# Kernel optimization log

Measured on AMD Instinct MI355X. Metric: run time of the kernel, lower is better.

## Reference

```python
import jax, jax.numpy as jnp
import numpy as np
import math

N = 8192
D = 512

def setup_inputs() -> dict:
    key = jax.random.key(0)
    k1, k2, k3, k4, k5 = jax.random.split(key, 5)
    x = jax.random.normal(k1, (N, D), dtype=jnp.float32)
    mask = jax.random.randint(k2, (N, N), 0, 2) == 1
    s = 1.0 / math.sqrt(D)
    Wq = jax.random.normal(k3, (D, D), dtype=jnp.float32) * s
    Wk = jax.random.normal(k4, (D, D), dtype=jnp.float32) * s
    Wv = jax.random.normal(k5, (D, D), dtype=jnp.float32) * s
    return {"x": x, "mask": mask, "Wq": Wq, "Wk": Wk, "Wv": Wv}

def reference(x, mask, Wq, Wk, Wv):
    d_model = x.shape[-1]
    # torch nn.Linear: y = x @ W^T
    Q = x @ Wq.T
    K = x @ Wk.T
    V = x @ Wv.T
    scores = (Q @ K.T) / jnp.sqrt(jnp.asarray(d_model, x.dtype))  # [N, N]
    scores = jnp.where(mask, jnp.asarray(-1e9, x.dtype), scores)
    # manual stable softmax, matching the original op sequence
    scores = jnp.exp(scores - jnp.max(scores, axis=1, keepdims=True))
    attn = scores / jnp.sum(scores, axis=-1, keepdims=True)
    cntx = attn @ V
    return (cntx, attn)
```

## Files before the change

### kernel.cpp

```cpp
#include <hip/hip_runtime.h>

#define NTOK 8192
#define DMODEL 512
#define NWORDS 128
#define ESTRIDE (2 * NTOK)

typedef _Float16 f16;
typedef _Float16 f16x4 __attribute__((ext_vector_type(4)));
typedef _Float16 f16x8 __attribute__((ext_vector_type(8)));
typedef float f32x4 __attribute__((ext_vector_type(4)));
typedef unsigned long long u64;

__device__ __forceinline__ void async_ld16(const void* g, void* l) {
  __builtin_amdgcn_global_load_lds((const __attribute__((address_space(1))) void*)g,
                                   (__attribute__((address_space(3))) void*)l, 16, 0, 0);
}

__global__ void pack_f16(const float* __restrict__ s, f16* __restrict__ d, int n) {
  int i = (blockIdx.x * 256 + threadIdx.x) * 4;
  if (i >= n) return;
  float4 v = *(const float4*)(s + i);
  f16x4 h; h.x = (f16)v.x; h.y = (f16)v.y; h.z = (f16)v.z; h.w = (f16)v.w;
  *(f16x4*)(d + i) = h;
}

__global__ __launch_bounds__(256) void pack_mask(const int* __restrict__ mask,
                                                 u64* __restrict__ bits) {
  int wave = (blockIdx.x * 256 + threadIdx.x) >> 6;
  int lane = threadIdx.x & 63;
  size_t W0 = (size_t)wave * 8;
#pragma unroll
  for (int i = 0; i < 8; ++i) {
    int m = mask[(W0 + i) * 64 + lane];
    u64 b = __ballot(m != 0);
    if (lane == 0) bits[W0 + i] = b;
  }
}

__global__ __launch_bounds__(256) void transpose_f16(const f16* __restrict__ src,
                                                     f16* __restrict__ dst) {
  __shared__ f16 T[64][72];
  int t = threadIdx.x;
  int tok0 = blockIdx.x * 64, d0 = blockIdx.y * 64;
#pragma unroll
  for (int i = 0; i < 2; ++i) {
    int row = (t >> 3) + i * 32;
    int col = (t & 7) * 8;
    f16x8 v = *(const f16x8*)(src + (size_t)(tok0 + row) * DMODEL + d0 + col);
    *(f16x8*)(&T[row][col]) = v;
  }
  __syncthreads();
#pragma unroll
  for (int i = 0; i < 2; ++i) {
    int od = (t >> 3) + i * 32;
    int ot = (t & 7) * 8;
    f16x8 v;
#pragma unroll
    for (int j = 0; j < 8; ++j) v[j] = T[ot + j][od];
    *(f16x8*)(dst + (size_t)(d0 + od) * NTOK + tok0 + ot) = v;
  }
}

__device__ __forceinline__ void stage128x64(const f16* G, int r0, int k0, int rs,
                                            f16* lds, int t) {
  int wv = t >> 6;
  const f16* g = G + (size_t)(r0 + (t >> 3)) * rs + k0 + (t & 7) * 8;
#pragma unroll
  for (int i = 0; i < 4; ++i)
    async_ld16(g + (size_t)i * 32 * rs, (char*)lds + i * 4096 + wv * 1024);
}

template <int RS>
__device__ __forceinline__ void gemm128(const f16* A, const f16* B, int m0, int n0,
                                        f16* As, f16* Bs, int t, f32x4 (&acc)[4][4]) {
  int lane = t & 63, wv = t >> 6, quad = lane >> 4, l15 = lane & 15;
  int m_off = (wv & 1) * 64, n_off = (wv >> 1) * 64;
  for (int kt = 0; kt < RS; kt += 64) {
    __syncthreads();
    stage128x64(A, m0, kt, RS, As, t);
    stage128x64(B, n0, kt, RS, Bs, t);
    __syncthreads();
#pragma unroll
    for (int ks = 0; ks < 2; ++ks) {
      f16x8 af[4], bf[4];
#pragma unroll
      for (int mt = 0; mt < 4; ++mt)
        af[mt] = *(const f16x8*)(As + (m_off + mt * 16 + l15) * 64 + ks * 32 + quad * 8);
#pragma unroll
      for (int nt = 0; nt < 4; ++nt)
        bf[nt] = *(const f16x8*)(Bs + (n_off + nt * 16 + l15) * 64 + ks * 32 + quad * 8);
#pragma unroll
      for (int mt = 0; mt < 4; ++mt)
#pragma unroll
        for (int nt = 0; nt < 4; ++nt)
          acc[mt][nt] = __builtin_amdgcn_mfma_f32_16x16x32_f16(af[mt], bf[nt], acc[mt][nt], 0, 0, 0);
    }
  }
}

__global__ __launch_bounds__(256) void qkv_gemm(const f16* __restrict__ X,
                                                const f16* __restrict__ Wall,
                                                f16* __restrict__ Out) {
  __shared__ f16 As[128 * 64];
  __shared__ f16 Bs[128 * 64];
  int t = threadIdx.x;
  int z = blockIdx.z;
  const f16* B = Wall + (size_t)z * DMODEL * DMODEL;
  f16* C = Out + (size_t)z * NTOK * DMODEL;
  int m0 = blockIdx.y * 128, n0 = blockIdx.x * 128;
  int lane = t & 63, wv = t >> 6, quad = lane >> 4, l15 = lane & 15;
  int m_off = (wv & 1) * 64, n_off = (wv >> 1) * 64;
  f32x4 acc[4][4] = {};
  gemm128<DMODEL>(X, B, m0, n0, As, Bs, t, acc);
#pragma unroll
  for (int mt = 0; mt < 4; ++mt)
#pragma unroll
    for (int nt = 0; nt < 4; ++nt)
#pragma unroll
      for (int r = 0; r < 4; ++r) {
        int row = m0 + m_off + mt * 16 + quad * 4 + r;
        int col = n0 + n_off + nt * 16 + l15;
        C[(size_t)row * DMODEL + col] = (f16)acc[mt][nt][r];
      }
}

__global__ __launch_bounds__(256) void scores2(const f16* __restrict__ Q,
                                               const f16* __restrict__ Kh,
                                               const u64* __restrict__ bits,
                                               f16* __restrict__ Eh,
                                               float* __restrict__ rowsum) {
  __shared__ f16 SM[128 * 128];
  f16* As = SM;
  f16* Bs = SM + 128 * 64;
  int t = threadIdx.x;
  int m0 = blockIdx.y * 128, n0 = blockIdx.x * 128;
  int lane = t & 63, wv = t >> 6, quad = lane >> 4, l15 = lane & 15;
  int m_off = (wv & 1) * 64, n_off = (wv >> 1) * 64;
  f32x4 acc[4][4] = {};
  gemm128<DMODEL>(Q, Kh, m0, n0, As, Bs, t, acc);
  const float scale = 0.044194173824159216f;
  __syncthreads();
#pragma unroll
  for (int mt = 0; mt < 4; ++mt)
#pragma unroll
    for (int r = 0; r < 4; ++r) {
      int lrow = m_off + mt * 16 + quad * 4 + r;
      int row = m0 + lrow;
      u64 w = bits[(size_t)row * NWORDS + ((n0 + n_off) >> 6)];
      float rs = 0.f;
#pragma unroll
      for (int nt = 0; nt < 4; ++nt) {
        float s = acc[mt][nt][r] * scale;
        float e = ((w >> (nt * 16 + l15)) & 1) ? 0.f : __expf(s);
        rs += e;
        int col = n_off + nt * 16 + l15;
        int phys = (((col >> 3) ^ (lrow & 15)) << 3) | (col & 7);
        SM[lrow * 128 + phys] = (f16)e;
      }
      rs += __shfl_xor(rs, 1);
      rs += __shfl_xor(rs, 2);
      rs += __shfl_xor(rs, 4);
      rs += __shfl_xor(rs, 8);
      if (l15 == 0) atomicAdd(&rowsum[row], rs);
    }
  __syncthreads();
#pragma unroll
  for (int p = 0; p < 8; ++p) {
    int lrow = p * 16 + (t >> 4);
    int cb = t & 15;
    f16x8 v = *(const f16x8*)(SM + lrow * 128 + ((cb ^ (lrow & 15)) << 3));
    *(f16x8*)(Eh + (size_t)(m0 + lrow) * ESTRIDE + n0 + cb * 8) = v;
  }
}

__global__ __launch_bounds__(512, 2) void pv_kernel(const f16* __restrict__ Eh,
                                                    const float* __restrict__ rowsum,
                                                    const f16* __restrict__ Vt,
                                                    float* __restrict__ cntx) {
  __shared__ f16 Es[128 * 32];
  __shared__ f16 Vs[512 * 32];
  int t = threadIdx.x;
  int r0 = blockIdx.x * 128;
  int k0 = blockIdx.y * 2048;
  int lane = t & 63, wv = t >> 6, quad = lane >> 4, l15 = lane & 15;
  int m_off = (wv & 1) * 64, n_off = (wv >> 1) * 128;
  f32x4 acc[4][8] = {};
  for (int kt = k0; kt < k0 + 2048; kt += 32) {
    __syncthreads();
    async_ld16(Eh + (size_t)(r0 + (t >> 2)) * ESTRIDE + kt + (t & 3) * 8,
               (char*)Es + wv * 1024);
#pragma unroll
    for (int i = 0; i < 4; ++i)
      async_ld16(Vt + (size_t)((i * 512 + t) >> 2) * NTOK + kt + (t & 3) * 8,
                 (char*)Vs + i * 8192 + wv * 1024);
    __syncthreads();
    f16x8 af[4], bf[8];
#pragma unroll
    for (int mt = 0; mt < 4; ++mt)
      af[mt] = *(const f16x8*)(Es + (m_off + mt * 16 + l15) * 32 + quad * 8);
#pragma unroll
    for (int nt = 0; nt < 8; ++nt)
      bf[nt] = *(const f16x8*)(Vs + (n_off + nt * 16 + l15) * 32 + quad * 8);
#pragma unroll
    for (int mt = 0; mt < 4; ++mt)
#pragma unroll
      for (int nt = 0; nt < 8; ++nt)
        acc[mt][nt] = __builtin_amdgcn_mfma_f32_16x16x32_f16(af[mt], bf[nt], acc[mt][nt], 0, 0, 0);
  }
#pragma unroll
  for (int mt = 0; mt < 4; ++mt)
#pragma unroll
    for (int r = 0; r < 4; ++r) {
      int row = r0 + m_off + mt * 16 + quad * 4 + r;
      float ri = 1.0f / rowsum[row];
#pragma unroll
      for (int nt = 0; nt < 8; ++nt) {
        int col = n_off + nt * 16 + l15;
        atomicAdd(&cntx[(size_t)row * DMODEL + col], acc[mt][nt][r] * ri);
      }
    }
}

__global__ __launch_bounds__(256) void expand_attn(float* __restrict__ attn,
                                                   const float* __restrict__ rowsum) {
  int t = threadIdx.x;
  int row = blockIdx.x * 4 + (t >> 6);
  size_t rb = (size_t)row * NTOK;
  const f16* Ehrow = (const f16*)(attn + rb);
  float ri = 1.0f / rowsum[row];
  int c0 = (t & 63) * 8;
  for (int c = NTOK - 512; c >= 0; c -= 512) {
    f16x8 v = *(const f16x8*)(Ehrow + c + c0);
    __syncthreads();
    float4 lo, hi;
    lo.x = (float)v[0] * ri; lo.y = (float)v[1] * ri;
    lo.z = (float)v[2] * ri; lo.w = (float)v[3] * ri;
    hi.x = (float)v[4] * ri; hi.y = (float)v[5] * ri;
    hi.z = (float)v[6] * ri; hi.w = (float)v[7] * ri;
    *(float4*)(attn + rb + c + c0) = lo;
    *(float4*)(attn + rb + c + c0 + 4) = hi;
  }
}

extern "C" void kernel_launch(void* const* d_in, const int* in_sizes, int n_in,
                              void* d_out, int out_size, void* d_ws, size_t ws_size,
                              hipStream_t stream) {
  const float* x  = (const float*)d_in[0];
  const int* mask = (const int*)d_in[1];
  const float* Wq = (const float*)d_in[2];
  const float* Wk = (const float*)d_in[3];
  const float* Wv = (const float*)d_in[4];
  float* cntx = (float*)d_out;
  float* attn = (float*)d_out + (size_t)NTOK * DMODEL;

  f16* xh = (f16*)d_ws;
  f16* Wh = xh + (size_t)NTOK * DMODEL;
  f16* QKV = Wh + (size_t)3 * DMODEL * DMODEL;
  f16* Qh = QKV;
  f16* Kh = QKV + (size_t)NTOK * DMODEL;
  f16* Vh = QKV + (size_t)2 * NTOK * DMODEL;
  f16* Vt = QKV + (size_t)3 * NTOK * DMODEL;
  float* rowsum = (float*)(Vt + (size_t)NTOK * DMODEL);

  u64* bits = (u64*)cntx;
  f16* Eh = (f16*)attn;

  hipMemsetAsync(rowsum, 0, NTOK * sizeof(float), stream);

  pack_f16<<<dim3(NTOK * DMODEL / 1024), 256, 0, stream>>>(x, xh, NTOK * DMODEL);
  pack_f16<<<dim3(DMODEL * DMODEL / 1024), 256, 0, stream>>>(Wq, Wh, DMODEL * DMODEL);
  pack_f16<<<dim3(DMODEL * DMODEL / 1024), 256, 0, stream>>>(Wk, Wh + DMODEL * DMODEL, DMODEL * DMODEL);
  pack_f16<<<dim3(DMODEL * DMODEL / 1024), 256, 0, stream>>>(Wv, Wh + 2 * DMODEL * DMODEL, DMODEL * DMODEL);
  pack_mask<<<dim3(NTOK * NWORDS / 8 / 4), 256, 0, stream>>>(mask, bits);

  qkv_gemm<<<dim3(DMODEL / 128, NTOK / 128, 3), 256, 0, stream>>>(xh, Wh, QKV);
  transpose_f16<<<dim3(NTOK / 64, DMODEL / 64), 256, 0, stream>>>(Vh, Vt);
  scores2<<<dim3(NTOK / 128, NTOK / 128), 256, 0, stream>>>(Qh, Kh, bits, Eh, rowsum);

  hipMemsetAsync(cntx, 0, (size_t)NTOK * DMODEL * sizeof(float), stream);
  pv_kernel<<<dim3(NTOK / 128, 4), 512, 0, stream>>>(Eh, rowsum, Vt, cntx);
  expand_attn<<<dim3(NTOK / 4), 256, 0, stream>>>(attn, rowsum);
}
```

Before: 896.7 us.

## Swizzle LDS tiles, widen PV k-step to 64, stage expand rows in LDS

Applies an XOR swizzle to the global-to-LDS staging and the matching fragment reads in the QKV GEMM and the PV kernel, to cut LDS bank conflicts. The PV kernel now stages 64-wide k tiles, which halves the number of barrier pairs per k range but uses twice the LDS. expand_attn now loads each whole f16 row into LDS once before widening it to f32 in place, which removes the per-chunk barrier and the reverse-order loop that had guarded against overwriting. The larger PV LDS footprint (80KB) and the 64KB of LDS per expand block may limit occupancy.

```diff
diff --git a/kernel.cpp b/kernel.cpp
--- a/kernel.cpp
+++ b/kernel.cpp
@@ -64,7 +64,8 @@
 __device__ __forceinline__ void stage128x64(const f16* G, int r0, int k0, int rs,
                                             f16* lds, int t) {
   int wv = t >> 6;
-  const f16* g = G + (size_t)(r0 + (t >> 3)) * rs + k0 + (t & 7) * 8;
+  int sw = (((t & 7) ^ ((t >> 3) & 7)) * 8);
+  const f16* g = G + (size_t)(r0 + (t >> 3)) * rs + k0 + sw;
 #pragma unroll
   for (int i = 0; i < 4; ++i)
     async_ld16(g + (size_t)i * 32 * rs, (char*)lds + i * 4096 + wv * 1024);
@@ -82,13 +83,14 @@
     __syncthreads();
 #pragma unroll
     for (int ks = 0; ks < 2; ++ks) {
+      int sl = (((ks << 2) | quad) ^ (l15 & 7)) * 8;
       f16x8 af[4], bf[4];
 #pragma unroll
       for (int mt = 0; mt < 4; ++mt)
-        af[mt] = *(const f16x8*)(As + (m_off + mt * 16 + l15) * 64 + ks * 32 + quad * 8);
+        af[mt] = *(const f16x8*)(As + (m_off + mt * 16 + l15) * 64 + sl);
 #pragma unroll
       for (int nt = 0; nt < 4; ++nt)
-        bf[nt] = *(const f16x8*)(Bs + (n_off + nt * 16 + l15) * 64 + ks * 32 + quad * 8);
+        bf[nt] = *(const f16x8*)(Bs + (n_off + nt * 16 + l15) * 64 + sl);
 #pragma unroll
       for (int mt = 0; mt < 4; ++mt)
 #pragma unroll
@@ -177,35 +179,42 @@
                                                     const float* __restrict__ rowsum,
                                                     const f16* __restrict__ Vt,
                                                     float* __restrict__ cntx) {
-  __shared__ f16 Es[128 * 32];
-  __shared__ f16 Vs[512 * 32];
+  __shared__ f16 Es[128 * 64];
+  __shared__ f16 Vs[512 * 64];
   int t = threadIdx.x;
   int r0 = blockIdx.x * 128;
   int k0 = blockIdx.y * 2048;
   int lane = t & 63, wv = t >> 6, quad = lane >> 4, l15 = lane & 15;
   int m_off = (wv & 1) * 64, n_off = (wv >> 1) * 128;
+  int sw = (((t & 7) ^ ((t >> 3) & 7)) * 8);
   f32x4 acc[4][8] = {};
-  for (int kt = k0; kt < k0 + 2048; kt += 32) {
-    __syncthreads();
-    async_ld16(Eh + (size_t)(r0 + (t >> 2)) * ESTRIDE + kt + (t & 3) * 8,
-               (char*)Es + wv * 1024);
-#pragma unroll
-    for (int i = 0; i < 4; ++i)
-      async_ld16(Vt + (size_t)((i * 512 + t) >> 2) * NTOK + kt + (t & 3) * 8,
+  for (int kt = k0; kt < k0 + 2048; kt += 64) {
+    __syncthreads();
+#pragma unroll
+    for (int i = 0; i < 2; ++i)
+      async_ld16(Eh + (size_t)(r0 + i * 64 + (t >> 3)) * ESTRIDE + kt + sw,
+                 (char*)Es + i * 8192 + wv * 1024);
+#pragma unroll
+    for (int i = 0; i < 8; ++i)
+      async_ld16(Vt + (size_t)(i * 64 + (t >> 3)) * NTOK + kt + sw,
                  (char*)Vs + i * 8192 + wv * 1024);
     __syncthreads();
-    f16x8 af[4], bf[8];
-#pragma unroll
-    for (int mt = 0; mt < 4; ++mt)
-      af[mt] = *(const f16x8*)(Es + (m_off + mt * 16 + l15) * 32 + quad * 8);
-#pragma unroll
-    for (int nt = 0; nt < 8; ++nt)
-      bf[nt] = *(const f16x8*)(Vs + (n_off + nt * 16 + l15) * 32 + quad * 8);
-#pragma unroll
-    for (int mt = 0; mt < 4; ++mt)
+#pragma unroll
+    for (int ks = 0; ks < 2; ++ks) {
+      int sl = (((ks << 2) | quad) ^ (l15 & 7)) * 8;
+      f16x8 af[4], bf[8];
+#pragma unroll
+      for (int mt = 0; mt < 4; ++mt)
+        af[mt] = *(const f16x8*)(Es + (m_off + mt * 16 + l15) * 64 + sl);
 #pragma unroll
       for (int nt = 0; nt < 8; ++nt)
-        acc[mt][nt] = __builtin_amdgcn_mfma_f32_16x16x32_f16(af[mt], bf[nt], acc[mt][nt], 0, 0, 0);
+        bf[nt] = *(const f16x8*)(Vs + (n_off + nt * 16 + l15) * 64 + sl);
+#pragma unroll
+      for (int mt = 0; mt < 4; ++mt)
+#pragma unroll
+        for (int nt = 0; nt < 8; ++nt)
+          acc[mt][nt] = __builtin_amdgcn_mfma_f32_16x16x32_f16(af[mt], bf[nt], acc[mt][nt], 0, 0, 0);
+    }
   }
 #pragma unroll
   for (int mt = 0; mt < 4; ++mt)
@@ -223,22 +232,27 @@
 
 __global__ __launch_bounds__(256) void expand_attn(float* __restrict__ attn,
                                                    const float* __restrict__ rowsum) {
-  int t = threadIdx.x;
-  int row = blockIdx.x * 4 + (t >> 6);
-  size_t rb = (size_t)row * NTOK;
-  const f16* Ehrow = (const f16*)(attn + rb);
+  __shared__ f16 B[4][8192];
+  int t = threadIdx.x;
+  int wv = t >> 6, lane = t & 63;
+  int row = blockIdx.x * 4 + wv;
+  const f16* src = (const f16*)(attn + (size_t)row * NTOK);
+#pragma unroll
+  for (int i = 0; i < 16; ++i)
+    async_ld16(src + i * 512 + lane * 8, (char*)&B[wv][0] + i * 1024);
+  __syncthreads();
   float ri = 1.0f / rowsum[row];
-  int c0 = (t & 63) * 8;
-  for (int c = NTOK - 512; c >= 0; c -= 512) {
-    f16x8 v = *(const f16x8*)(Ehrow + c + c0);
-    __syncthreads();
+  float* dst = attn + (size_t)row * NTOK;
+#pragma unroll
+  for (int c = 0; c < NTOK; c += 512) {
+    f16x8 v = *(const f16x8*)(&B[wv][c + lane * 8]);
     float4 lo, hi;
     lo.x = (float)v[0] * ri; lo.y = (float)v[1] * ri;
     lo.z = (float)v[2] * ri; lo.w = (float)v[3] * ri;
     hi.x = (float)v[4] * ri; hi.y = (float)v[5] * ri;
     hi.z = (float)v[6] * ri; hi.w = (float)v[7] * ri;
-    *(float4*)(attn + rb + c + c0) = lo;
-    *(float4*)(attn + rb + c + c0 + 4) = hi;
+    *(float4*)(dst + c + lane * 8) = lo;
+    *(float4*)(dst + c + lane * 8 + 4) = hi;
   }
 }
 
```

New measurement: 852.2 us. 1.05x faster.
